# Kernel optimization log

Measured on AMD Instinct MI355X. Metric: run time of the kernel, lower is better.

## Reference

```python
import jax, jax.numpy as jnp
import numpy as np

NUM_WIRES = 14
LAYERS = 3
PPL = 3
BATCH = 1024
DIM = 2 ** NUM_WIRES


def setup_inputs() -> dict:
    key = jax.random.key(0)
    k1, k2, k3, k4, k5 = jax.random.split(key, 5)
    sr = jax.random.normal(k1, (BATCH, DIM), jnp.float32)
    si = jax.random.normal(k2, (BATCH, DIM), jnp.float32)
    norm = jnp.sqrt(jnp.sum(sr * sr + si * si, axis=1, keepdims=True))
    sr, si = sr / norm, si / norm  # normalized amplitude-encoded states
    weights = jax.random.normal(k3, (LAYERS, PPL, NUM_WIRES), jnp.float32)
    head_w = jax.random.normal(k4, (1, NUM_WIRES), jnp.float32) / np.sqrt(NUM_WIRES)
    head_b = jax.random.normal(k5, (1,), jnp.float32) * 0.01
    return {"state_real": sr, "state_imag": si, "weights": weights,
            "head_w": head_w, "head_b": head_b}


def _apply_ry_all(st, angles):
    # st: (B,)+(2,)*n complex; apply RY(angles[q]) on each wire q (RYs on distinct wires commute)
    half = angles * 0.5
    c, s = jnp.cos(half), jnp.sin(half)
    for q in range(NUM_WIRES):
        ax = 1 + q
        a0 = jnp.take(st, 0, axis=ax)
        a1 = jnp.take(st, 1, axis=ax)
        n0 = c[q] * a0 - s[q] * a1
        n1 = s[q] * a0 + c[q] * a1
        st = jnp.stack([n0, n1], axis=ax)
    return st


def _apply_cnot(st, ctrl, tgt):
    # flip target axis only where control bit == 1
    ctrl_ax, tgt_ax = 1 + ctrl, 1 + tgt
    flipped = jnp.flip(st, axis=tgt_ax)
    mask_shape = [1] * (NUM_WIRES + 1)
    mask_shape[ctrl_ax] = 2
    mask = (jnp.arange(2).reshape(mask_shape) == 1)
    return jnp.where(mask, flipped, st)


def _circuit(state, weights):
    # state: (B, DIM) complex64 -> PauliZ expvals (B, NUM_WIRES)
    st = state.reshape((-1,) + (2,) * NUM_WIRES)
    for l in range(LAYERS):
        # sequential RY(w[l,p,q]) for p=0..PPL-1 on wire q compose to RY(sum_p w[l,p,q])
        ang = jnp.sum(weights[l], axis=0)  # (NUM_WIRES,)
        st = _apply_ry_all(st, ang)
        for j in range(NUM_WIRES):
            st = _apply_cnot(st, j, (j + 1) % NUM_WIRES)
    probs = st.real ** 2 + st.imag ** 2  # (B,)+(2,)*n
    probs = probs.reshape(-1, DIM)
    idx = jnp.arange(DIM)
    # PennyLane convention: wire 0 is the most significant bit
    bits = (idx[None, :] >> (NUM_WIRES - 1 - jnp.arange(NUM_WIRES))[:, None]) & 1  # (n, DIM)
    signs = (1 - 2 * bits).astype(probs.dtype)
    return probs @ signs.T  # (B, n)


def reference(state_real, state_imag, weights, head_w, head_b):
    state = jax.lax.complex(state_real, state_imag)
    feats = _circuit(state, weights)  # (B, NUM_WIRES)
    return feats @ head_w[0] + head_b[0]  # (B,)
```

## Files before the change

### kernel.cpp

```cpp
#include <hip/hip_runtime.h>

typedef unsigned int u32;
typedef float v2f __attribute__((ext_vector_type(2)));

#define DIM 16384
#define NT  512

__host__ __device__ constexpr u32 swz0(u32 d) {
    u32 b1 = (d >> 4) & 1u;
    u32 b2 = (d >> 7) & 1u;
    u32 b3 = ((d >> 6) ^ (d >> 8)) & 1u;
    return d ^ (b1 << 1) ^ (b2 << 2) ^ (b3 << 3);
}

__host__ __device__ constexpr u32 mmap(u32 y) {
    u32 s = y;
    s ^= s >> 1; s ^= s >> 2; s ^= s >> 4; s ^= s >> 8;
    return (s & 0x1FFFu) | (((s ^ (y >> 13)) & 1u) << 13);
}

__device__ __forceinline__ void rot2(v2f& a0, v2f& a1, v2f cv, v2f sv, v2f nsv) {
    v2f t0 = cv * a0;
    v2f t1 = cv * a1;
    v2f n0 = __builtin_elementwise_fma(nsv, a1, t0);
    v2f n1 = __builtin_elementwise_fma(sv,  a0, t1);
    a0 = n0; a1 = n1;
}

template<int D>
__device__ __forceinline__ void gate32(v2f (&am)[32], float c, float s) {
    v2f cv = {c, c}, sv = {s, s}, nsv = {-s, -s};
    #pragma unroll
    for (int r = 0; r < 32; ++r) if (!(r & D)) rot2(am[r], am[r | D], cv, sv, nsv);
}

template<int L>
__device__ __forceinline__ void passA(int tid, float* smem, v2f (&am)[32]) {
    float4* stv = (float4*)smem;
    const float* angC = smem + 32768;
    const float* angS = smem + 32768 + 48;
    u32 sbase = swz0((u32)tid << 2);
    if (L > 0) {
        #pragma unroll
        for (int h = 0; h < 8; ++h) {
            #pragma unroll
            for (int m = 0; m < 2; ++m) {
                u32 idx = (sbase ^ swz0(((u32)h << 11) | ((u32)m << 1))) >> 1;
                float4 v = stv[idx];
                int r = h * 4 + m * 2;
                am[r].x     = v.x; am[r].y     = v.y;
                am[r + 1].x = v.z; am[r + 1].y = v.w;
            }
        }
    }
    gate32< 1>(am, angC[L * 16 +  0], angS[L * 16 +  0]);
    gate32< 2>(am, angC[L * 16 +  1], angS[L * 16 +  1]);
    gate32< 4>(am, angC[L * 16 + 11], angS[L * 16 + 11]);
    gate32< 8>(am, angC[L * 16 + 12], angS[L * 16 + 12]);
    gate32<16>(am, angC[L * 16 + 13], angS[L * 16 + 13]);
    #pragma unroll
    for (int h = 0; h < 8; ++h) {
        #pragma unroll
        for (int m = 0; m < 2; ++m) {
            u32 idx = (sbase ^ swz0(((u32)h << 11) | ((u32)m << 1))) >> 1;
            int r = h * 4 + m * 2;
            stv[idx] = make_float4(am[r].x, am[r].y, am[r + 1].x, am[r + 1].y);
        }
    }
    __syncthreads();
}

template<int L>
__device__ __forceinline__ void passB(int tid, float* smem, v2f (&am)[32]) {
    float2* st2 = (float2*)smem;
    const float* angC = smem + 32768;
    const float* angS = smem + 32768 + 48;
    u32 ybase = ((u32)tid & 63u) | (((u32)tid >> 6) << 11);
    u32 sbase = swz0(ybase);
    #pragma unroll
    for (int j = 0; j < 32; ++j) {
        float2 v = st2[sbase ^ swz0((u32)j << 6)];
        am[j].x = v.x; am[j].y = v.y;
    }
    gate32< 1>(am, angC[L * 16 +  6], angS[L * 16 +  6]);
    gate32< 2>(am, angC[L * 16 +  7], angS[L * 16 +  7]);
    gate32< 4>(am, angC[L * 16 +  8], angS[L * 16 +  8]);
    gate32< 8>(am, angC[L * 16 +  9], angS[L * 16 +  9]);
    gate32<16>(am, angC[L * 16 + 10], angS[L * 16 + 10]);
    #pragma unroll
    for (int j = 0; j < 32; ++j) {
        st2[sbase ^ swz0((u32)j << 6)] = make_float2(am[j].x, am[j].y);
    }
    __syncthreads();
}

template<int L>
__device__ __forceinline__ void passC(int tid, float* smem, v2f (&am)[32],
                                      float& acc, float W0) {
    float2* st2 = (float2*)smem;
    float4* stv = (float4*)smem;
    const float* angC  = smem + 32768;
    const float* angS  = smem + 32768 + 48;
    const float* lutLo = smem + 32768 + 96;
    const float* lutHi = smem + 32768 + 96 + 128;
    u32 ybase = (((u32)tid & 1u) << 1) | (((u32)tid >> 1) << 6);
    u32 sbase = swz0(ybase);
    #pragma unroll
    for (int h = 0; h < 16; ++h) {
        u32 idx = (sbase ^ swz0((u32)h << 2)) >> 1;
        float4 v = stv[idx];
        int r = h * 2;
        am[r].x     = v.x; am[r].y     = v.y;
        am[r + 1].x = v.z; am[r + 1].y = v.w;
    }
    gate32< 2>(am, angC[L * 16 + 2], angS[L * 16 + 2]);
    gate32< 4>(am, angC[L * 16 + 3], angS[L * 16 + 3]);
    gate32< 8>(am, angC[L * 16 + 4], angS[L * 16 + 4]);
    gate32<16>(am, angC[L * 16 + 5], angS[L * 16 + 5]);
    if (L < 2) {
        __syncthreads();
        u32 pbase = swz0(mmap(ybase));
        #pragma unroll
        for (int h = 0; h < 16; ++h) {
            #pragma unroll
            for (int q = 0; q < 2; ++q) {
                u32 slot = pbase ^ swz0(mmap(((u32)h << 2) | (u32)q));
                int r = h * 2 + q;
                st2[slot] = make_float2(am[r].x, am[r].y);
            }
        }
        __syncthreads();
    } else {
        u32 myb = mmap(ybase);
        #pragma unroll
        for (int h = 0; h < 16; ++h) {
            #pragma unroll
            for (int q = 0; q < 2; ++q) {
                u32 yp = myb ^ mmap(((u32)h << 2) | (u32)q);
                int r = h * 2 + q;
                float p  = fmaf(am[r].x, am[r].x, am[r].y * am[r].y);
                float wv = W0 - 2.0f * (lutLo[yp & 127u] + lutHi[yp >> 7]);
                acc = fmaf(wv, p, acc);
            }
        }
    }
}

__global__ __launch_bounds__(NT, 2) void qsim_kernel(
    const float* __restrict__ sreal, const float* __restrict__ simag,
    const float* __restrict__ wts,   const float* __restrict__ hw,
    const float* __restrict__ hb,    float* __restrict__ out)
{
    extern __shared__ float smem[];
    float* angC   = smem + 32768;
    float* angS   = angC + 48;
    float* lutLo  = angS + 48;
    float* lutHi  = lutLo + 128;
    float* redbuf = lutHi + 128;

    int tid = threadIdx.x;
    int b   = blockIdx.x;

    const float4* pr = (const float4*)(sreal + (size_t)b * DIM);
    const float4* pi = (const float4*)(simag + (size_t)b * DIM);
    float4 vr[8], vi[8];
    #pragma unroll
    for (int h = 0; h < 8; ++h) {
        vr[h] = pr[(h << 9) | tid];
        vi[h] = pi[(h << 9) | tid];
    }

    if (tid < 42) {
        int l = tid / 14, bb = tid % 14, q = 13 - bb;
        float a = 0.5f * (wts[l * 42 + q] + wts[l * 42 + 14 + q] + wts[l * 42 + 28 + q]);
        angC[l * 16 + bb] = cosf(a);
        angS[l * 16 + bb] = sinf(a);
    } else if (tid >= 64 && tid < 192) {
        int i = tid - 64;
        float ssum = 0.f;
        for (int bb = 0; bb < 7; ++bb) if ((i >> bb) & 1) ssum += hw[13 - bb];
        lutLo[i] = ssum;
    } else if (tid >= 192 && tid < 320) {
        int i = tid - 192;
        float ssum = 0.f;
        for (int bb = 0; bb < 7; ++bb) if ((i >> bb) & 1) ssum += hw[6 - bb];
        lutHi[i] = ssum;
    }

    v2f am[32];
    #pragma unroll
    for (int h = 0; h < 8; ++h) {
        am[h * 4 + 0].x = vr[h].x; am[h * 4 + 0].y = vi[h].x;
        am[h * 4 + 1].x = vr[h].y; am[h * 4 + 1].y = vi[h].y;
        am[h * 4 + 2].x = vr[h].z; am[h * 4 + 2].y = vi[h].z;
        am[h * 4 + 3].x = vr[h].w; am[h * 4 + 3].y = vi[h].w;
    }

    __syncthreads();
    float W0  = lutLo[127] + lutHi[127];
    float acc = 0.f;

    passA<0>(tid, smem, am);
    passB<0>(tid, smem, am);
    passC<0>(tid, smem, am, acc, W0);
    passA<1>(tid, smem, am);
    passB<1>(tid, smem, am);
    passC<1>(tid, smem, am, acc, W0);
    passA<2>(tid, smem, am);
    passB<2>(tid, smem, am);
    passC<2>(tid, smem, am, acc, W0);

    #pragma unroll
    for (int off = 32; off > 0; off >>= 1) acc += __shfl_xor(acc, off, 64);
    if ((tid & 63) == 0) redbuf[tid >> 6] = acc;
    __syncthreads();
    if (tid == 0) {
        float tot = hb[0];
        #pragma unroll
        for (int i = 0; i < 8; ++i) tot += redbuf[i];
        out[b] = tot;
    }
}

extern "C" void kernel_launch(void* const* d_in, const int* in_sizes, int n_in,
                              void* d_out, int out_size, void* d_ws, size_t ws_size,
                              hipStream_t stream)
{
    const float* sreal = (const float*)d_in[0];
    const float* simag = (const float*)d_in[1];
    const float* wts   = (const float*)d_in[2];
    const float* hw    = (const float*)d_in[3];
    const float* hb    = (const float*)d_in[4];
    float* out = (float*)d_out;

    int batch = in_sizes[0] / DIM;
    size_t smem_bytes = (32768 + 48 + 48 + 128 + 128 + 16) * sizeof(float);

    (void)hipFuncSetAttribute((const void*)qsim_kernel,
                              hipFuncAttributeMaxDynamicSharedMemorySize, (int)smem_bytes);
    qsim_kernel<<<dim3(batch), dim3(NT), smem_bytes, stream>>>(sreal, simag, wts, hw, hb, out);
}
```

Measured before the change: 220.3 us.

## Halve LDS footprint by exchanging state in two half-rounds, raise occupancy

The full 128KB shared-memory state buffer is replaced by a 64KB buffer, and each inter-pass transpose becomes a two-phase exchange. Half the threads (or half the data) go through the buffer per phase, and temporary registers hold the staged half. This is meant to let more blocks fit per CU (launch bounds raised from 2 to 4) so latency is better hidden. In exchange it doubles the barriers per exchange, adds 16 extra v2f registers under a tighter register budget with spill risk, and adds remapping logic such as parity selection in exCA.

```diff
diff --git a/kernel.cpp b/kernel.cpp
--- a/kernel.cpp
+++ b/kernel.cpp
@@ -6,17 +6,20 @@
 #define DIM 16384
 #define NT  512
 
-__host__ __device__ constexpr u32 swz0(u32 d) {
-    u32 b1 = (d >> 4) & 1u;
-    u32 b2 = (d >> 7) & 1u;
-    u32 b3 = ((d >> 6) ^ (d >> 8)) & 1u;
-    return d ^ (b1 << 1) ^ (b2 << 2) ^ (b3 << 3);
+__host__ __device__ constexpr u32 fslot(u32 s) {
+    return s ^ (((s >> 4) & 1u) << 1)
+             ^ ((((s >> 6) ^ (s >> 8)) & 1u) << 2)
+             ^ (((s >> 7) & 1u) << 3);
 }
 
 __host__ __device__ constexpr u32 mmap(u32 y) {
     u32 s = y;
     s ^= s >> 1; s ^= s >> 2; s ^= s >> 4; s ^= s >> 8;
     return (s & 0x1FFFu) | (((s ^ (y >> 13)) & 1u) << 13);
+}
+
+__host__ __device__ constexpr u32 bcmap(u32 y) {
+    return (y & 0x3FFu) | (((y >> 11) & 7u) << 10);
 }
 
 __device__ __forceinline__ void rot2(v2f& a0, v2f& a1, v2f cv, v2f sv, v2f nsv) {
@@ -34,125 +37,173 @@
     for (int r = 0; r < 32; ++r) if (!(r & D)) rot2(am[r], am[r | D], cv, sv, nsv);
 }
 
+__device__ __forceinline__ void exAB(int tid, float* buf, v2f (&am)[32], v2f (&tmp)[16]) {
+    float4* b4 = (float4*)buf;
+    float2* b2 = (float2*)buf;
+    u32 sA = fslot((u32)tid << 2);
+    u32 sB = fslot(((u32)tid & 63u) | ((((u32)tid >> 6) & 3u) << 11));
+    int myv = (tid >> 8) & 1;
+    #pragma unroll
+    for (int h = 0; h < 4; ++h)
+        #pragma unroll
+        for (int m = 0; m < 2; ++m) {
+            u32 f4 = (sA ^ fslot(((u32)h << 11) | ((u32)m << 1))) >> 1;
+            int r = h * 4 + m * 2;
+            b4[f4] = make_float4(am[r].x, am[r].y, am[r + 1].x, am[r + 1].y);
+        }
+    __syncthreads();
+    if (myv == 0) {
+        #pragma unroll
+        for (int j = 0; j < 16; ++j) {
+            float2 t = b2[sB ^ fslot((u32)j << 6)]; am[j].x = t.x; am[j].y = t.y;
+        }
+        #pragma unroll
+        for (int j = 16; j < 32; ++j) {
+            float2 t = b2[sB ^ fslot((u32)j << 6)]; tmp[j - 16].x = t.x; tmp[j - 16].y = t.y;
+        }
+    }
+    __syncthreads();
+    #pragma unroll
+    for (int h = 4; h < 8; ++h)
+        #pragma unroll
+        for (int m = 0; m < 2; ++m) {
+            u32 f4 = (sA ^ fslot((((u32)h & 3u) << 11) | ((u32)m << 1))) >> 1;
+            int r = h * 4 + m * 2;
+            b4[f4] = make_float4(am[r].x, am[r].y, am[r + 1].x, am[r + 1].y);
+        }
+    __syncthreads();
+    if (myv == 1) {
+        #pragma unroll
+        for (int j = 0; j < 32; ++j) {
+            float2 t = b2[sB ^ fslot((u32)j << 6)]; am[j].x = t.x; am[j].y = t.y;
+        }
+    } else {
+        #pragma unroll
+        for (int j = 0; j < 16; ++j) am[16 + j] = tmp[j];
+    }
+    __syncthreads();
+}
+
+__device__ __forceinline__ void exBC(int tid, float* buf, v2f (&am)[32], v2f (&tmp)[16]) {
+    float4* b4 = (float4*)buf;
+    float2* b2 = (float2*)buf;
+    u32 sW = fslot(bcmap(((u32)tid & 63u) | (((u32)tid >> 6) << 11)));
+    u32 sR = fslot(bcmap((((u32)tid & 1u) << 1) | (((u32)tid >> 1) << 6)));
+    int myv = (tid >> 5) & 1;
+    #pragma unroll
+    for (int j = 0; j < 16; ++j)
+        b2[sW ^ fslot((u32)j << 6)] = make_float2(am[j].x, am[j].y);
+    __syncthreads();
+    if (myv == 0) {
+        #pragma unroll
+        for (int h = 0; h < 8; ++h) {
+            float4 v = b4[(sR ^ fslot((u32)h << 2)) >> 1];
+            am[h * 2].x = v.x; am[h * 2].y = v.y; am[h * 2 + 1].x = v.z; am[h * 2 + 1].y = v.w;
+        }
+        #pragma unroll
+        for (int h = 8; h < 16; ++h) {
+            float4 v = b4[(sR ^ fslot((u32)h << 2)) >> 1];
+            int r = (h - 8) * 2;
+            tmp[r].x = v.x; tmp[r].y = v.y; tmp[r + 1].x = v.z; tmp[r + 1].y = v.w;
+        }
+    }
+    __syncthreads();
+    #pragma unroll
+    for (int j = 16; j < 32; ++j)
+        b2[sW ^ fslot((u32)(j & 15) << 6)] = make_float2(am[j].x, am[j].y);
+    __syncthreads();
+    if (myv == 1) {
+        #pragma unroll
+        for (int h = 0; h < 16; ++h) {
+            float4 v = b4[(sR ^ fslot((u32)h << 2)) >> 1];
+            am[h * 2].x = v.x; am[h * 2].y = v.y; am[h * 2 + 1].x = v.z; am[h * 2 + 1].y = v.w;
+        }
+    } else {
+        #pragma unroll
+        for (int j = 0; j < 16; ++j) am[16 + j] = tmp[j];
+    }
+    __syncthreads();
+}
+
+__device__ __forceinline__ void exCA(int tid, float* buf, v2f (&am)[32], v2f (&tmp)[16]) {
+    float4* b4 = (float4*)buf;
+    float2* b2 = (float2*)buf;
+    u32 ybase = (((u32)tid & 1u) << 1) | (((u32)tid >> 1) << 6);
+    u32 sW = fslot(mmap(ybase) & 0x1FFFu);
+    u32 sA = fslot((u32)tid << 2);
+    u32 P = (u32)__builtin_popcount(ybase & 0x1FFFu) & 1u;
+    #pragma unroll
+    for (int h = 0; h < 16; ++h) {
+        u32 pc = (u32)(__builtin_popcount((unsigned)h) & 1);
+        u32 q = P ^ pc;
+        u32 slot = sW ^ fslot(mmap((u32)h << 2) & 0x1FFFu) ^ q;
+        v2f val = q ? am[h * 2 + 1] : am[h * 2];
+        b2[slot] = make_float2(val.x, val.y);
+    }
+    __syncthreads();
+    #pragma unroll
+    for (int h = 0; h < 4; ++h)
+        #pragma unroll
+        for (int m = 0; m < 2; ++m) {
+            float4 v = b4[(sA ^ fslot(((u32)h << 11) | ((u32)m << 1))) >> 1];
+            int r = h * 4 + m * 2;
+            tmp[r].x = v.x; tmp[r].y = v.y; tmp[r + 1].x = v.z; tmp[r + 1].y = v.w;
+        }
+    __syncthreads();
+    #pragma unroll
+    for (int h = 0; h < 16; ++h) {
+        u32 pc = (u32)(__builtin_popcount((unsigned)h) & 1);
+        u32 q = P ^ pc ^ 1u;
+        u32 slot = sW ^ fslot(mmap((u32)h << 2) & 0x1FFFu) ^ q;
+        v2f val = q ? am[h * 2 + 1] : am[h * 2];
+        b2[slot] = make_float2(val.x, val.y);
+    }
+    __syncthreads();
+    #pragma unroll
+    for (int h = 4; h < 8; ++h)
+        #pragma unroll
+        for (int m = 0; m < 2; ++m) {
+            float4 v = b4[(sA ^ fslot((((u32)h & 3u) << 11) | ((u32)m << 1))) >> 1];
+            int r = h * 4 + m * 2;
+            am[r].x = v.x; am[r].y = v.y; am[r + 1].x = v.z; am[r + 1].y = v.w;
+        }
+    #pragma unroll
+    for (int r = 0; r < 16; ++r) am[r] = tmp[r];
+    __syncthreads();
+}
+
 template<int L>
-__device__ __forceinline__ void passA(int tid, float* smem, v2f (&am)[32]) {
-    float4* stv = (float4*)smem;
-    const float* angC = smem + 32768;
-    const float* angS = smem + 32768 + 48;
-    u32 sbase = swz0((u32)tid << 2);
-    if (L > 0) {
-        #pragma unroll
-        for (int h = 0; h < 8; ++h) {
-            #pragma unroll
-            for (int m = 0; m < 2; ++m) {
-                u32 idx = (sbase ^ swz0(((u32)h << 11) | ((u32)m << 1))) >> 1;
-                float4 v = stv[idx];
-                int r = h * 4 + m * 2;
-                am[r].x     = v.x; am[r].y     = v.y;
-                am[r + 1].x = v.z; am[r + 1].y = v.w;
-            }
-        }
-    }
+__device__ __forceinline__ void gatesA(const float* angC, const float* angS, v2f (&am)[32]) {
     gate32< 1>(am, angC[L * 16 +  0], angS[L * 16 +  0]);
     gate32< 2>(am, angC[L * 16 +  1], angS[L * 16 +  1]);
     gate32< 4>(am, angC[L * 16 + 11], angS[L * 16 + 11]);
     gate32< 8>(am, angC[L * 16 + 12], angS[L * 16 + 12]);
     gate32<16>(am, angC[L * 16 + 13], angS[L * 16 + 13]);
-    #pragma unroll
-    for (int h = 0; h < 8; ++h) {
-        #pragma unroll
-        for (int m = 0; m < 2; ++m) {
-            u32 idx = (sbase ^ swz0(((u32)h << 11) | ((u32)m << 1))) >> 1;
-            int r = h * 4 + m * 2;
-            stv[idx] = make_float4(am[r].x, am[r].y, am[r + 1].x, am[r + 1].y);
-        }
-    }
-    __syncthreads();
-}
-
+}
 template<int L>
-__device__ __forceinline__ void passB(int tid, float* smem, v2f (&am)[32]) {
-    float2* st2 = (float2*)smem;
-    const float* angC = smem + 32768;
-    const float* angS = smem + 32768 + 48;
-    u32 ybase = ((u32)tid & 63u) | (((u32)tid >> 6) << 11);
-    u32 sbase = swz0(ybase);
-    #pragma unroll
-    for (int j = 0; j < 32; ++j) {
-        float2 v = st2[sbase ^ swz0((u32)j << 6)];
-        am[j].x = v.x; am[j].y = v.y;
-    }
+__device__ __forceinline__ void gatesB(const float* angC, const float* angS, v2f (&am)[32]) {
     gate32< 1>(am, angC[L * 16 +  6], angS[L * 16 +  6]);
     gate32< 2>(am, angC[L * 16 +  7], angS[L * 16 +  7]);
     gate32< 4>(am, angC[L * 16 +  8], angS[L * 16 +  8]);
     gate32< 8>(am, angC[L * 16 +  9], angS[L * 16 +  9]);
     gate32<16>(am, angC[L * 16 + 10], angS[L * 16 + 10]);
-    #pragma unroll
-    for (int j = 0; j < 32; ++j) {
-        st2[sbase ^ swz0((u32)j << 6)] = make_float2(am[j].x, am[j].y);
-    }
-    __syncthreads();
-}
-
+}
 template<int L>
-__device__ __forceinline__ void passC(int tid, float* smem, v2f (&am)[32],
-                                      float& acc, float W0) {
-    float2* st2 = (float2*)smem;
-    float4* stv = (float4*)smem;
-    const float* angC  = smem + 32768;
-    const float* angS  = smem + 32768 + 48;
-    const float* lutLo = smem + 32768 + 96;
-    const float* lutHi = smem + 32768 + 96 + 128;
-    u32 ybase = (((u32)tid & 1u) << 1) | (((u32)tid >> 1) << 6);
-    u32 sbase = swz0(ybase);
-    #pragma unroll
-    for (int h = 0; h < 16; ++h) {
-        u32 idx = (sbase ^ swz0((u32)h << 2)) >> 1;
-        float4 v = stv[idx];
-        int r = h * 2;
-        am[r].x     = v.x; am[r].y     = v.y;
-        am[r + 1].x = v.z; am[r + 1].y = v.w;
-    }
+__device__ __forceinline__ void gatesC(const float* angC, const float* angS, v2f (&am)[32]) {
     gate32< 2>(am, angC[L * 16 + 2], angS[L * 16 + 2]);
     gate32< 4>(am, angC[L * 16 + 3], angS[L * 16 + 3]);
     gate32< 8>(am, angC[L * 16 + 4], angS[L * 16 + 4]);
     gate32<16>(am, angC[L * 16 + 5], angS[L * 16 + 5]);
-    if (L < 2) {
-        __syncthreads();
-        u32 pbase = swz0(mmap(ybase));
-        #pragma unroll
-        for (int h = 0; h < 16; ++h) {
-            #pragma unroll
-            for (int q = 0; q < 2; ++q) {
-                u32 slot = pbase ^ swz0(mmap(((u32)h << 2) | (u32)q));
-                int r = h * 2 + q;
-                st2[slot] = make_float2(am[r].x, am[r].y);
-            }
-        }
-        __syncthreads();
-    } else {
-        u32 myb = mmap(ybase);
-        #pragma unroll
-        for (int h = 0; h < 16; ++h) {
-            #pragma unroll
-            for (int q = 0; q < 2; ++q) {
-                u32 yp = myb ^ mmap(((u32)h << 2) | (u32)q);
-                int r = h * 2 + q;
-                float p  = fmaf(am[r].x, am[r].x, am[r].y * am[r].y);
-                float wv = W0 - 2.0f * (lutLo[yp & 127u] + lutHi[yp >> 7]);
-                acc = fmaf(wv, p, acc);
-            }
-        }
-    }
-}
-
-__global__ __launch_bounds__(NT, 2) void qsim_kernel(
+}
+
+__global__ __launch_bounds__(NT, 4) void qsim_kernel(
     const float* __restrict__ sreal, const float* __restrict__ simag,
     const float* __restrict__ wts,   const float* __restrict__ hw,
     const float* __restrict__ hb,    float* __restrict__ out)
 {
     extern __shared__ float smem[];
-    float* angC   = smem + 32768;
+    float* buf    = smem;
+    float* angC   = smem + 16384;
     float* angS   = angC + 48;
     float* lutLo  = angS + 48;
     float* lutHi  = lutLo + 128;
@@ -188,6 +239,7 @@
     }
 
     v2f am[32];
+    v2f tmp[16];
     #pragma unroll
     for (int h = 0; h < 8; ++h) {
         am[h * 4 + 0].x = vr[h].x; am[h * 4 + 0].y = vi[h].x;
@@ -200,15 +252,31 @@
     float W0  = lutLo[127] + lutHi[127];
     float acc = 0.f;
 
-    passA<0>(tid, smem, am);
-    passB<0>(tid, smem, am);
-    passC<0>(tid, smem, am, acc, W0);
-    passA<1>(tid, smem, am);
-    passB<1>(tid, smem, am);
-    passC<1>(tid, smem, am, acc, W0);
-    passA<2>(tid, smem, am);
-    passB<2>(tid, smem, am);
-    passC<2>(tid, smem, am, acc, W0);
+    gatesA<0>(angC, angS, am); exAB(tid, buf, am, tmp);
+    gatesB<0>(angC, angS, am); exBC(tid, buf, am, tmp);
+    gatesC<0>(angC, angS, am); exCA(tid, buf, am, tmp);
+    gatesA<1>(angC, angS, am); exAB(tid, buf, am, tmp);
+    gatesB<1>(angC, angS, am); exBC(tid, buf, am, tmp);
+    gatesC<1>(angC, angS, am); exCA(tid, buf, am, tmp);
+    gatesA<2>(angC, angS, am); exAB(tid, buf, am, tmp);
+    gatesB<2>(angC, angS, am); exBC(tid, buf, am, tmp);
+    gatesC<2>(angC, angS, am);
+
+    {
+        u32 ybase = (((u32)tid & 1u) << 1) | (((u32)tid >> 1) << 6);
+        u32 myb = mmap(ybase);
+        #pragma unroll
+        for (int h = 0; h < 16; ++h) {
+            #pragma unroll
+            for (int q = 0; q < 2; ++q) {
+                u32 yp = myb ^ mmap(((u32)h << 2) | (u32)q);
+                int r = h * 2 + q;
+                float p  = fmaf(am[r].x, am[r].x, am[r].y * am[r].y);
+                float wv = W0 - 2.0f * (lutLo[yp & 127u] + lutHi[yp >> 7]);
+                acc = fmaf(wv, p, acc);
+            }
+        }
+    }
 
     #pragma unroll
     for (int off = 32; off > 0; off >>= 1) acc += __shfl_xor(acc, off, 64);
@@ -234,7 +302,7 @@
     float* out = (float*)d_out;
 
     int batch = in_sizes[0] / DIM;
-    size_t smem_bytes = (32768 + 48 + 48 + 128 + 128 + 16) * sizeof(float);
+    size_t smem_bytes = (16384 + 48 + 48 + 128 + 128 + 16) * sizeof(float);
 
     (void)hipFuncSetAttribute((const void*)qsim_kernel,
                               hipFuncAttributeMaxDynamicSharedMemorySize, (int)smem_bytes);
```

Measured after the change: 841.5 us. 282% more time.
